# Kernel tuning notes

Hardware: AMD Instinct MI355X
Metric: run time of the kernel (lower is better)

Reference implementation:

```python
import jax, jax.numpy as jnp
import numpy as np

B, T, F, H, M = 64, 512, 32, 512, 20
O = (F + 2) * M  # (n_features + 2) * num_mixtures = 680


def _lstm_cell(x, h, c, w_ih, w_hh, b_ih, b_hh):
    # torch.nn.LSTMCell: gates ordered [i, f, g, o]
    gates = x @ w_ih.T + h @ w_hh.T + b_ih + b_hh
    i, f, g, o = jnp.split(gates, 4, axis=-1)
    i = jax.nn.sigmoid(i)
    f = jax.nn.sigmoid(f)
    g = jnp.tanh(g)
    o = jax.nn.sigmoid(o)
    c_new = f * c + i * g
    h_new = o * jnp.tanh(c_new)
    return h_new, c_new


def setup_inputs() -> dict:
    key = jax.random.key(0)
    ks = jax.random.split(key, 9)
    s1 = 1.0 / np.sqrt(H)  # torch LSTMCell init: U(-1/sqrt(hidden), 1/sqrt(hidden))
    s2 = 1.0 / np.sqrt(O)
    u = lambda k, shape, s: jax.random.uniform(k, shape, jnp.float32, -s, s)
    return {
        "data": jax.random.normal(ks[0], (B, T * F), jnp.float32),
        "W_ih1": u(ks[1], (4 * H, F), s1),
        "W_hh1": u(ks[2], (4 * H, H), s1),
        "b_ih1": u(ks[3], (4 * H,), s1),
        "b_hh1": u(ks[4], (4 * H,), s1),
        "W_ih2": u(ks[5], (4 * O, H), s2),
        "W_hh2": u(ks[6], (4 * O, O), s2),
        "b_ih2": u(ks[7], (4 * O,), s2),
        "b_hh2": u(ks[8], (4 * O,), s2),
    }


def reference(data, W_ih1, W_hh1, b_ih1, b_hh1, W_ih2, W_hh2, b_ih2, b_hh2):
    n_feat = W_ih1.shape[1]
    hid = W_hh1.shape[1]
    out_dim = W_hh2.shape[1]
    batch = data.shape[0]
    t_steps = data.shape[1] // n_feat
    xs = data.reshape(batch, t_steps, n_feat).transpose(1, 0, 2)  # (T, B, F)

    h1 = jnp.zeros((batch, hid), data.dtype)
    c1 = jnp.zeros((batch, hid), data.dtype)
    h2 = jnp.zeros((batch, out_dim), data.dtype)
    c2 = jnp.zeros((batch, out_dim), data.dtype)

    def step(carry, x_t):
        h1, c1, h2, c2 = carry
        h1, c1 = _lstm_cell(x_t, h1, c1, W_ih1, W_hh1, b_ih1, b_hh1)
        # NOTE: original feeds lstm1's CELL state c1 into lstm2, and collects
        # lstm2's CELL state (`output`) as the per-step output.
        h2, c2 = _lstm_cell(c1, h2, c2, W_ih2, W_hh2, b_ih2, b_hh2)
        return (h1, c1, h2, c2), c2

    _, outs = jax.lax.scan(step, (h1, c1, h2, c2), xs)  # (T, B, O)
    return outs.transpose(1, 0, 2)  # (B, T, O), matches torch.stack(outputs, 1)
```

## Files before the change

### kernel.cpp

```cpp
#include <hip/hip_runtime.h>
#include <math.h>

#define BB 64
#define TT 512
#define FF 32
#define HH 512
#define OO 680

typedef _Float16 half8 __attribute__((ext_vector_type(8)));
typedef float f32x4 __attribute__((ext_vector_type(4)));

#define H1SLAB 65536u
#define C1SLAB 65536u
#define H2SLAB 90112u
#define H1S_OFF 0u
#define C1S_OFF 131072u
#define H2S_OFF 262144u
#define BAR_OFF 442368u
#define MEMSET_BYTES 444928u

#define L1B  16
#define NBLK 59
#define LDS_BYTES 159744u

__device__ __forceinline__ float sigf(float x) { return 1.f / (1.f + expf(-x)); }

__device__ __forceinline__ unsigned long long aload8(const void* p) {
    return __hip_atomic_load((const unsigned long long*)p, __ATOMIC_RELAXED, __HIP_MEMORY_SCOPE_AGENT);
}
__device__ __forceinline__ void astore8(void* p, unsigned long long v) {
    __hip_atomic_store((unsigned long long*)p, v, __ATOMIC_RELAXED, __HIP_MEMORY_SCOPE_AGENT);
}
__device__ __forceinline__ half8 ld_act(const char* p) {
    union { unsigned long long u[2]; half8 h; } t;
    t.u[0] = aload8(p); t.u[1] = aload8(p + 8);
    return t.h;
}
__device__ __forceinline__ unsigned pack2h(float a, float b) {
    union { _Float16 h[2]; unsigned u; } t;
    t.h[0] = (_Float16)a; t.h[1] = (_Float16)b; return t.u;
}
__device__ __forceinline__ unsigned long long pack4h(float a, float b, float c, float d) {
    union { _Float16 h[4]; unsigned long long u; } t;
    t.h[0] = (_Float16)a; t.h[1] = (_Float16)b; t.h[2] = (_Float16)c; t.h[3] = (_Float16)d;
    return t.u;
}

__device__ __forceinline__ void gridbar(unsigned* bar, int blk, unsigned gen) {
    __syncthreads();
    if (threadIdx.x == 0) {
        const int x = blk & 7;
        const unsigned gsz = (x < 3) ? 8u : 7u;
        unsigned* cnt = bar + x * 32;
        const unsigned a = __hip_atomic_fetch_add(cnt, 1u, __ATOMIC_RELAXED, __HIP_MEMORY_SCOPE_AGENT);
        if (a == gen * gsz - 1u)
            __hip_atomic_store(bar + 256 + x * 32, gen, __ATOMIC_RELAXED, __HIP_MEMORY_SCOPE_AGENT);
        for (;;) {
            unsigned ok = 1u;
            #pragma unroll
            for (int r = 0; r < 8; ++r)
                ok &= (__hip_atomic_load(bar + 256 + r * 32, __ATOMIC_RELAXED, __HIP_MEMORY_SCOPE_AGENT) >= gen) ? 1u : 0u;
            if (ok) break;
            __builtin_amdgcn_s_sleep(1);
        }
    }
    __syncthreads();
}

#define MFMA4(B, AT) \
    acc0 = __builtin_amdgcn_mfma_f32_16x16x32_f16(*(const half8*)((AT)       ), (B), acc0, 0, 0, 0); \
    acc1 = __builtin_amdgcn_mfma_f32_16x16x32_f16(*(const half8*)((AT) + 1024), (B), acc1, 0, 0, 0); \
    acc2 = __builtin_amdgcn_mfma_f32_16x16x32_f16(*(const half8*)((AT) + 2048), (B), acc2, 0, 0, 0); \
    acc3 = __builtin_amdgcn_mfma_f32_16x16x32_f16(*(const half8*)((AT) + 3072), (B), acc3, 0, 0, 0);

__global__ __launch_bounds__(512, 1)
void rnn_mfma(const float* __restrict__ data,
    const float* __restrict__ Wih1, const float* __restrict__ Whh1,
    const float* __restrict__ bih1, const float* __restrict__ bhh1,
    const float* __restrict__ Wih2, const float* __restrict__ Whh2,
    const float* __restrict__ bih2, const float* __restrict__ bhh2,
    char* __restrict__ wsb, float* __restrict__ out)
{
    extern __shared__ char lds[];
    const int tid = threadIdx.x, wv = tid >> 6, l = tid & 63;
    const int hi = l >> 4, lo = l & 15;
    const int blk = blockIdx.x;
    const bool isL1 = blk < L1B;
    unsigned* bar = (unsigned*)(wsb + BAR_OFF);
    const int bfrag = wv & 3;
    const int b = bfrag * 16 + lo;
    const int c0 = isL1 ? blk * 32 : (blk - L1B) * 16;

    if (isL1) {
        for (int u = tid; u < 136 * 256; u += 512) {
            const int tile = u >> 8, w = u & 255;
            const int ll = w >> 2, jj = w & 3;
            const int ks = tile >> 3, rest = tile & 7;
            const int gate = rest >> 1, chi = rest & 1;
            const int col = c0 + chi * 16 + (ll & 15);
            const int row = gate * HH + col;
            const int kk = ks * 32 + (ll >> 4) * 8 + jj * 2;
            const float v0 = (kk < FF)     ? Wih1[(size_t)row * FF + kk]     : Whh1[(size_t)row * HH + kk - FF];
            const float v1 = (kk + 1 < FF) ? Wih1[(size_t)row * FF + kk + 1] : Whh1[(size_t)row * HH + kk + 1 - FF];
            ((unsigned*)lds)[tile * 256 + w] = pack2h(v0, v1);
        }
    } else {
        for (int u = tid; u < 152 * 256; u += 512) {
            const int tile = u >> 8, w = u & 255;
            const int ll = w >> 2, jj = w & 3;
            const int ks = tile >> 2, gate = tile & 3;
            const int col = c0 + (ll & 15);
            const int kk = ks * 32 + (ll >> 4) * 8 + jj * 2;
            float v0 = 0.f, v1 = 0.f;
            if (col < OO) {
                if (kk < HH) v0 = Wih2[((size_t)gate * OO + col) * HH + kk];
                else if (kk < 1192) v0 = Whh2[((size_t)gate * OO + col) * OO + kk - HH];
                if (kk + 1 < HH) v1 = Wih2[((size_t)gate * OO + col) * HH + kk + 1];
                else if (kk + 1 < 1192) v1 = Whh2[((size_t)gate * OO + col) * OO + kk + 1 - HH];
            }
            ((unsigned*)lds)[tile * 256 + w] = pack2h(v0, v1);
        }
    }
    __syncthreads();

    float bs[2][4][4];
    if (wv < 4) {
        if (isL1) {
            #pragma unroll
            for (int chi = 0; chi < 2; ++chi)
                #pragma unroll
                for (int r = 0; r < 4; ++r) {
                    const int col = c0 + chi * 16 + hi * 4 + r;
                    #pragma unroll
                    for (int g = 0; g < 4; ++g)
                        bs[chi][r][g] = bih1[g * HH + col] + bhh1[g * HH + col];
                }
        } else {
            #pragma unroll
            for (int r = 0; r < 4; ++r) {
                const int col = c0 + hi * 4 + r;
                const bool ok = col < OO;
                #pragma unroll
                for (int g = 0; g < 4; ++g)
                    bs[0][r][g] = ok ? (bih2[g * OO + col] + bhh2[g * OO + col]) : 0.f;
            }
        }
    }

    const int gh = wv >> 2;
    float cr[8] = {0.f,0.f,0.f,0.f,0.f,0.f,0.f,0.f};
    f32x4 (*part1)[4][64] = (f32x4(*)[4][64])(lds + 136 * 1024);
    f32x4* part2 = (f32x4*)(lds + 152 * 1024);

    f32x4 pend = {0,0,0,0};
    float* pendP = nullptr;

    for (int s = 0; s <= TT; ++s) {
        const int A = s & 1, Bx = A ^ 1;
        const bool active = isL1 ? (s < TT) : (s >= 1);
        f32x4 acc0 = {0,0,0,0}, acc1 = {0,0,0,0}, acc2 = {0,0,0,0}, acc3 = {0,0,0,0};

        if (active) {
            if (isL1) {
                {
                    const float* xp = data + (size_t)b * (TT * FF) + (size_t)s * FF + hi * 8;
                    const float4 xa = *(const float4*)xp;
                    const float4 xb = *(const float4*)(xp + 4);
                    half8 bxf;
                    bxf[0] = (_Float16)xa.x; bxf[1] = (_Float16)xa.y;
                    bxf[2] = (_Float16)xa.z; bxf[3] = (_Float16)xa.w;
                    bxf[4] = (_Float16)xb.x; bxf[5] = (_Float16)xb.y;
                    bxf[6] = (_Float16)xb.z; bxf[7] = (_Float16)xb.w;
                    const char* at = lds + (size_t)(gh * 4) * 1024 + (size_t)l * 16;
                    MFMA4(bxf, at);
                }
                const char* h1p = wsb + H1S_OFF + (size_t)A * H1SLAB + (size_t)l * 16;
                #pragma unroll
                for (int ks = 1; ks <= 16; ++ks) {
                    const half8 bf = ld_act(h1p + (size_t)(((ks - 1) * 4 + bfrag)) * 1024);
                    const char* at = lds + (size_t)(ks * 8 + gh * 4) * 1024 + (size_t)l * 16;
                    MFMA4(bf, at);
                }
            } else {
                if (gh == 0) {
                    if (pendP) { __builtin_nontemporal_store(pend, (f32x4*)pendP); pendP = nullptr; }
                    const char* c1p = wsb + C1S_OFF + (size_t)A * C1SLAB + (size_t)l * 16;
                    #pragma unroll
                    for (int ks = 0; ks < 16; ++ks) {
                        const half8 bf = ld_act(c1p + (size_t)(ks * 4 + bfrag) * 1024);
                        const char* at = lds + (size_t)ks * 4096 + (size_t)l * 16;
                        MFMA4(bf, at);
                    }
                    const char* h2p = wsb + H2S_OFF + (size_t)Bx * H2SLAB + (size_t)l * 16;
                    #pragma unroll
                    for (int ks = 16; ks < 19; ++ks) {
                        const half8 bf = ld_act(h2p + (size_t)((ks - 16) * 4 + bfrag) * 1024);
                        const char* at = lds + (size_t)ks * 4096 + (size_t)l * 16;
                        MFMA4(bf, at);
                    }
                } else {
                    const char* h2p = wsb + H2S_OFF + (size_t)Bx * H2SLAB + (size_t)l * 16;
                    #pragma unroll
                    for (int ks = 19; ks < 38; ++ks) {
                        const half8 bf = ld_act(h2p + (size_t)((ks - 16) * 4 + bfrag) * 1024);
                        const char* at = lds + (size_t)ks * 4096 + (size_t)l * 16;
                        MFMA4(bf, at);
                    }
                }
            }
        }

        if (isL1) {
            if (active) {
                if (wv >= 4) {
                    part1[wv - 4][0][l] = acc0; part1[wv - 4][1][l] = acc1;
                    part1[wv - 4][2][l] = acc2; part1[wv - 4][3][l] = acc3;
                }
                __syncthreads();
                if (wv < 4) {
                    #pragma unroll
                    for (int chi = 0; chi < 2; ++chi) {
                        const f32x4 o0 = (chi == 0) ? acc0 : acc1;
                        const f32x4 o1 = (chi == 0) ? acc2 : acc3;
                        const f32x4 p0 = part1[wv][chi][l];
                        const f32x4 p1 = part1[wv][2 + chi][l];
                        float cn[4], hn[4];
                        #pragma unroll
                        for (int r = 0; r < 4; ++r) {
                            const float ig = sigf(o0[r] + bs[chi][r][0]);
                            const float fg = sigf(o1[r] + bs[chi][r][1]);
                            const float gg = tanhf(p0[r] + bs[chi][r][2]);
                            const float og = sigf(p1[r] + bs[chi][r][3]);
                            const float c = fg * cr[chi * 4 + r] + ig * gg;
                            cr[chi * 4 + r] = c;
                            cn[r] = c; hn[r] = og * tanhf(c);
                        }
                        const int cc = c0 + chi * 16 + hi * 4;
                        const size_t aoff = (size_t)(((cc >> 5) * 4 + wv)) * 1024
                                          + (size_t)((((cc >> 3) & 3) * 16 + lo)) * 16
                                          + (size_t)((hi & 1) * 8);
                        astore8(wsb + H1S_OFF + (size_t)Bx * H1SLAB + aoff, pack4h(hn[0], hn[1], hn[2], hn[3]));
                        astore8(wsb + C1S_OFF + (size_t)Bx * C1SLAB + aoff, pack4h(cn[0], cn[1], cn[2], cn[3]));
                    }
                }
            }
        } else {
            if (active) {
                f32x4 pr0 = {0,0,0,0}, pr1 = {0,0,0,0}, pr2 = {0,0,0,0}, pr3 = {0,0,0,0};
                if (wv >= 4) part2[(wv - 4) * 64 + l] = acc0;
                __syncthreads();
                if (wv < 4) pr0 = part2[wv * 64 + l];
                __syncthreads();
                if (wv >= 4) part2[(wv - 4) * 64 + l] = acc1;
                __syncthreads();
                if (wv < 4) pr1 = part2[wv * 64 + l];
                __syncthreads();
                if (wv >= 4) part2[(wv - 4) * 64 + l] = acc2;
                __syncthreads();
                if (wv < 4) pr2 = part2[wv * 64 + l];
                __syncthreads();
                if (wv >= 4) part2[(wv - 4) * 64 + l] = acc3;
                __syncthreads();
                if (wv < 4) pr3 = part2[wv * 64 + l];
                if (wv < 4) {
                    const int u = s - 1;
                    float cn[4], hn[4];
                    #pragma unroll
                    for (int r = 0; r < 4; ++r) {
                        const float ig = sigf(acc0[r] + pr0[r] + bs[0][r][0]);
                        const float fg = sigf(acc1[r] + pr1[r] + bs[0][r][1]);
                        const float gg = tanhf(acc2[r] + pr2[r] + bs[0][r][2]);
                        const float og = sigf(acc3[r] + pr3[r] + bs[0][r][3]);
                        const float c = fg * cr[r] + ig * gg;
                        cr[r] = c;
                        cn[r] = c; hn[r] = og * tanhf(c);
                    }
                    const int cc = c0 + hi * 4;
                    if (cc < OO) {
                        pend[0] = cn[0]; pend[1] = cn[1]; pend[2] = cn[2]; pend[3] = cn[3];
                        pendP = out + (size_t)b * (TT * OO) + (size_t)u * OO + cc;
                        const size_t aoff = (size_t)(((cc >> 5) * 4 + wv)) * 1024
                                          + (size_t)((((cc >> 3) & 3) * 16 + lo)) * 16
                                          + (size_t)((hi & 1) * 8);
                        astore8(wsb + H2S_OFF + (size_t)A * H2SLAB + aoff, pack4h(hn[0], hn[1], hn[2], hn[3]));
                    }
                }
            }
        }
        gridbar(bar, blk, (unsigned)(s + 1));
    }

    if (!isL1 && wv < 4 && pendP)
        __builtin_nontemporal_store(pend, (f32x4*)pendP);
}

extern "C" void kernel_launch(void* const* d_in, const int* in_sizes, int n_in,
                              void* d_out, int out_size, void* d_ws, size_t ws_size,
                              hipStream_t stream)
{
    const float* data = (const float*)d_in[0];
    const float* Wih1 = (const float*)d_in[1];
    const float* Whh1 = (const float*)d_in[2];
    const float* bih1 = (const float*)d_in[3];
    const float* bhh1 = (const float*)d_in[4];
    const float* Wih2 = (const float*)d_in[5];
    const float* Whh2 = (const float*)d_in[6];
    const float* bih2 = (const float*)d_in[7];
    const float* bhh2 = (const float*)d_in[8];
    float* out = (float*)d_out;
    char* wsb  = (char*)d_ws;

    hipFuncSetAttribute((const void*)rnn_mfma, hipFuncAttributeMaxDynamicSharedMemorySize, (int)LDS_BYTES);
    hipMemsetAsync(wsb, 0, MEMSET_BYTES, stream);
    rnn_mfma<<<NBLK, 512, LDS_BYTES, stream>>>(data,
                                               Wih1, Whh1, bih1, bhh1,
                                               Wih2, Whh2, bih2, bhh2,
                                               wsb, out);
}
```

Baseline: 4.895 ms.

## Replace global grid barrier with layer-wise flag sync and 4-deep c1 ring

Replaces the per-step grid-wide barrier with separate producer/consumer counters and flags for layer-1 and layer-2 blocks. Layer 1 can now run up to three steps ahead of layer 2 through a 4-deep ring buffer for c1. Blocks shrink to 256 threads, so each wave does the full K reduction itself and the LDS partial-sum exchange with its extra __syncthreads is gone. The aim is to cut barrier latency and intra-block sync overhead on the serial recurrence, at the cost of more serial MFMA work per wave and busy-wait spinning without sleep.

Measured after the change: 4.495 ms. 8.2% less time.

```diff
diff --git a/kernel.cpp b/kernel.cpp
--- a/kernel.cpp
+++ b/kernel.cpp
@@ -15,13 +15,18 @@
 #define H2SLAB 90112u
 #define H1S_OFF 0u
 #define C1S_OFF 131072u
-#define H2S_OFF 262144u
-#define BAR_OFF 442368u
-#define MEMSET_BYTES 444928u
+#define H2S_OFF 393216u
+#define BAR_OFF 573440u
+#define MEMSET_BYTES 576000u
 
 #define L1B  16
 #define NBLK 59
-#define LDS_BYTES 159744u
+#define LDS_BYTES 155648u
+
+#define L1CNT(g) ((g)*32)
+#define L1FLG    64
+#define L2CNT(g) (96 + (g)*32)
+#define L2FLG    352
 
 __device__ __forceinline__ float sigf(float x) { return 1.f / (1.f + expf(-x)); }
 
@@ -30,6 +35,9 @@
 }
 __device__ __forceinline__ void astore8(void* p, unsigned long long v) {
     __hip_atomic_store((unsigned long long*)p, v, __ATOMIC_RELAXED, __HIP_MEMORY_SCOPE_AGENT);
+}
+__device__ __forceinline__ void astore32(unsigned* p, unsigned v) {
+    __hip_atomic_store(p, v, __ATOMIC_RELAXED, __HIP_MEMORY_SCOPE_AGENT);
 }
 __device__ __forceinline__ half8 ld_act(const char* p) {
     union { unsigned long long u[2]; half8 h; } t;
@@ -45,35 +53,29 @@
     t.h[0] = (_Float16)a; t.h[1] = (_Float16)b; t.h[2] = (_Float16)c; t.h[3] = (_Float16)d;
     return t.u;
 }
-
-__device__ __forceinline__ void gridbar(unsigned* bar, int blk, unsigned gen) {
-    __syncthreads();
-    if (threadIdx.x == 0) {
-        const int x = blk & 7;
-        const unsigned gsz = (x < 3) ? 8u : 7u;
-        unsigned* cnt = bar + x * 32;
-        const unsigned a = __hip_atomic_fetch_add(cnt, 1u, __ATOMIC_RELAXED, __HIP_MEMORY_SCOPE_AGENT);
-        if (a == gen * gsz - 1u)
-            __hip_atomic_store(bar + 256 + x * 32, gen, __ATOMIC_RELAXED, __HIP_MEMORY_SCOPE_AGENT);
-        for (;;) {
-            unsigned ok = 1u;
-            #pragma unroll
-            for (int r = 0; r < 8; ++r)
-                ok &= (__hip_atomic_load(bar + 256 + r * 32, __ATOMIC_RELAXED, __HIP_MEMORY_SCOPE_AGENT) >= gen) ? 1u : 0u;
-            if (ok) break;
-            __builtin_amdgcn_s_sleep(1);
-        }
-    }
-    __syncthreads();
-}
-
-#define MFMA4(B, AT) \
-    acc0 = __builtin_amdgcn_mfma_f32_16x16x32_f16(*(const half8*)((AT)       ), (B), acc0, 0, 0, 0); \
-    acc1 = __builtin_amdgcn_mfma_f32_16x16x32_f16(*(const half8*)((AT) + 1024), (B), acc1, 0, 0, 0); \
-    acc2 = __builtin_amdgcn_mfma_f32_16x16x32_f16(*(const half8*)((AT) + 2048), (B), acc2, 0, 0, 0); \
-    acc3 = __builtin_amdgcn_mfma_f32_16x16x32_f16(*(const half8*)((AT) + 3072), (B), acc3, 0, 0, 0);
-
-__global__ __launch_bounds__(512, 1)
+__device__ __forceinline__ unsigned minL1(const unsigned* bar) {
+    const unsigned long long v = aload8(bar + L1FLG);
+    const unsigned a = (unsigned)v, b = (unsigned)(v >> 32);
+    return a < b ? a : b;
+}
+__device__ __forceinline__ unsigned minL2(const unsigned* bar) {
+    const unsigned long long v0 = aload8(bar + L2FLG);
+    const unsigned long long v1 = aload8(bar + L2FLG + 2);
+    const unsigned long long v2 = aload8(bar + L2FLG + 4);
+    const unsigned long long v3 = aload8(bar + L2FLG + 6);
+    unsigned m = (unsigned)v0;
+    unsigned x;
+    x = (unsigned)(v0 >> 32); m = x < m ? x : m;
+    x = (unsigned)v1;         m = x < m ? x : m;
+    x = (unsigned)(v1 >> 32); m = x < m ? x : m;
+    x = (unsigned)v2;         m = x < m ? x : m;
+    x = (unsigned)(v2 >> 32); m = x < m ? x : m;
+    x = (unsigned)v3;         m = x < m ? x : m;
+    x = (unsigned)(v3 >> 32); m = x < m ? x : m;
+    return m;
+}
+
+__global__ __launch_bounds__(256, 1)
 void rnn_mfma(const float* __restrict__ data,
     const float* __restrict__ Wih1, const float* __restrict__ Whh1,
     const float* __restrict__ bih1, const float* __restrict__ bhh1,
@@ -85,14 +87,13 @@
     const int tid = threadIdx.x, wv = tid >> 6, l = tid & 63;
     const int hi = l >> 4, lo = l & 15;
     const int blk = blockIdx.x;
-    const bool isL1 = blk < L1B;
     unsigned* bar = (unsigned*)(wsb + BAR_OFF);
-    const int bfrag = wv & 3;
+    const int bfrag = wv;
     const int b = bfrag * 16 + lo;
-    const int c0 = isL1 ? blk * 32 : (blk - L1B) * 16;
-
-    if (isL1) {
-        for (int u = tid; u < 136 * 256; u += 512) {
+
+    if (blk < L1B) {
+        const int c0 = blk * 32;
+        for (int u = tid; u < 136 * 256; u += 256) {
             const int tile = u >> 8, w = u & 255;
             const int ll = w >> 2, jj = w & 3;
             const int ks = tile >> 3, rest = tile & 7;
@@ -104,8 +105,86 @@
             const float v1 = (kk + 1 < FF) ? Wih1[(size_t)row * FF + kk + 1] : Whh1[(size_t)row * HH + kk + 1 - FF];
             ((unsigned*)lds)[tile * 256 + w] = pack2h(v0, v1);
         }
+        __syncthreads();
+
+        float bs[2][4][4];
+        #pragma unroll
+        for (int chi = 0; chi < 2; ++chi)
+            #pragma unroll
+            for (int r = 0; r < 4; ++r) {
+                const int col = c0 + chi * 16 + hi * 4 + r;
+                #pragma unroll
+                for (int g = 0; g < 4; ++g)
+                    bs[chi][r][g] = bih1[g * HH + col] + bhh1[g * HH + col];
+            }
+        float cr[8] = {0.f,0.f,0.f,0.f,0.f,0.f,0.f,0.f};
+
+        for (int s = 0; s < TT; ++s) {
+            const int pr = s & 1;
+            const float* xp = data + (size_t)b * (TT * FF) + (size_t)s * FF + hi * 8;
+            const float4 xa = *(const float4*)xp;
+            const float4 xb4 = *(const float4*)(xp + 4);
+            if (s > 0) {
+                if (tid == 0) { while (minL1(bar) < (unsigned)s) {} }
+                __syncthreads();
+            }
+            half8 bx;
+            bx[0] = (_Float16)xa.x; bx[1] = (_Float16)xa.y; bx[2] = (_Float16)xa.z; bx[3] = (_Float16)xa.w;
+            bx[4] = (_Float16)xb4.x; bx[5] = (_Float16)xb4.y; bx[6] = (_Float16)xb4.z; bx[7] = (_Float16)xb4.w;
+
+            f32x4 acc[8];
+            #pragma unroll
+            for (int a = 0; a < 8; ++a) acc[a] = (f32x4){0.f,0.f,0.f,0.f};
+            #pragma unroll
+            for (int a = 0; a < 8; ++a)
+                acc[a] = __builtin_amdgcn_mfma_f32_16x16x32_f16(*(const half8*)(lds + (size_t)a * 1024 + (size_t)l * 16), bx, acc[a], 0, 0, 0);
+            const char* h1p = wsb + H1S_OFF + (size_t)pr * H1SLAB + (size_t)l * 16;
+            #pragma unroll
+            for (int ks = 1; ks <= 16; ++ks) {
+                const half8 bf = ld_act(h1p + (size_t)((ks - 1) * 4 + bfrag) * 1024);
+                #pragma unroll
+                for (int a = 0; a < 8; ++a)
+                    acc[a] = __builtin_amdgcn_mfma_f32_16x16x32_f16(*(const half8*)(lds + (size_t)(ks * 8 + a) * 1024 + (size_t)l * 16), bf, acc[a], 0, 0, 0);
+            }
+            if (s > 3) {
+                if (tid == 0) { while (minL2(bar) < (unsigned)(s - 3)) {} }
+                __syncthreads();
+            }
+            char* h1w = wsb + H1S_OFF + (size_t)(pr ^ 1) * H1SLAB;
+            char* c1w = wsb + C1S_OFF + (size_t)(s & 3) * C1SLAB;
+            #pragma unroll
+            for (int chi = 0; chi < 2; ++chi) {
+                const int cc = c0 + chi * 16 + hi * 4;
+                float cn[4], hn[4];
+                #pragma unroll
+                for (int r = 0; r < 4; ++r) {
+                    const float ig = sigf(acc[0 + chi][r] + bs[chi][r][0]);
+                    const float fg = sigf(acc[2 + chi][r] + bs[chi][r][1]);
+                    const float gg = tanhf(acc[4 + chi][r] + bs[chi][r][2]);
+                    const float og = sigf(acc[6 + chi][r] + bs[chi][r][3]);
+                    const float c = fg * cr[chi * 4 + r] + ig * gg;
+                    cr[chi * 4 + r] = c;
+                    cn[r] = c; hn[r] = og * tanhf(c);
+                }
+                const size_t aoff = (size_t)((cc >> 5) * 4 + bfrag) * 1024
+                                  + (size_t)((((cc >> 3) & 3) * 16 + lo)) * 16
+                                  + (size_t)(cc & 7) * 2;
+                astore8(h1w + aoff, pack4h(hn[0], hn[1], hn[2], hn[3]));
+                astore8(c1w + aoff, pack4h(cn[0], cn[1], cn[2], cn[3]));
+            }
+            __syncthreads();
+            if (tid == 0) {
+                const int g = blk & 1;
+                const unsigned e = (unsigned)(s + 1);
+                const unsigned a2 = __hip_atomic_fetch_add(bar + L1CNT(g), 1u, __ATOMIC_RELAXED, __HIP_MEMORY_SCOPE_AGENT);
+                if (a2 == e * 8u - 1u) astore32(bar + L1FLG + g, e);
+            }
+        }
     } else {
-        for (int u = tid; u < 152 * 256; u += 512) {
+        const int idx = blk - L1B, c0 = idx * 16;
+        const int grp = idx & 7;
+        const unsigned gsz = (grp < 3) ? 6u : 5u;
+        for (int u = tid; u < 152 * 256; u += 256) {
             const int tile = u >> 8, w = u & 255;
             const int ll = w >> 2, jj = w & 3;
             const int ks = tile >> 2, gate = tile & 3;
@@ -120,178 +199,78 @@
             }
             ((unsigned*)lds)[tile * 256 + w] = pack2h(v0, v1);
         }
+        __syncthreads();
+
+        const int cc = c0 + hi * 4;
+        float bs[4][4];
+        #pragma unroll
+        for (int r = 0; r < 4; ++r) {
+            const int col = cc + r;
+            const bool ok = col < OO;
+            #pragma unroll
+            for (int g = 0; g < 4; ++g)
+                bs[r][g] = ok ? (bih2[g * OO + col] + bhh2[g * OO + col]) : 0.f;
+        }
+        float cr[4] = {0.f,0.f,0.f,0.f};
+
+        for (int t = 1; t <= TT; ++t) {
+            if (tid == 0) { while (minL1(bar) < (unsigned)t) {} }
+            __syncthreads();
+            const char* c1p = wsb + C1S_OFF + (size_t)((t - 1) & 3) * C1SLAB + (size_t)l * 16;
+            half8 bcs[16];
+            #pragma unroll
+            for (int ks = 0; ks < 16; ++ks) bcs[ks] = ld_act(c1p + (size_t)(ks * 4 + bfrag) * 1024);
+            if (t > 1) {
+                if (tid == 0) { while (minL2(bar) < (unsigned)(t - 1)) {} }
+                __syncthreads();
+            }
+            const char* h2p = wsb + H2S_OFF + (size_t)((t & 1) ^ 1) * H2SLAB + (size_t)l * 16;
+            half8 bhs[22];
+            #pragma unroll
+            for (int ks = 0; ks < 22; ++ks) bhs[ks] = ld_act(h2p + (size_t)(ks * 4 + bfrag) * 1024);
+            f32x4 acc[4];
+            #pragma unroll
+            for (int g = 0; g < 4; ++g) acc[g] = (f32x4){0.f,0.f,0.f,0.f};
+            #pragma unroll
+            for (int ks = 0; ks < 16; ++ks) {
+                #pragma unroll
+                for (int g = 0; g < 4; ++g)
+                    acc[g] = __builtin_amdgcn_mfma_f32_16x16x32_f16(*(const half8*)(lds + (size_t)(ks * 4 + g) * 1024 + (size_t)l * 16), bcs[ks], acc[g], 0, 0, 0);
+            }
+            #pragma unroll
+            for (int ks = 0; ks < 22; ++ks) {
+                #pragma unroll
+                for (int g = 0; g < 4; ++g)
+                    acc[g] = __builtin_amdgcn_mfma_f32_16x16x32_f16(*(const half8*)(lds + (size_t)((16 + ks) * 4 + g) * 1024 + (size_t)l * 16), bhs[ks], acc[g], 0, 0, 0);
+            }
+            if (cc < OO) {
+                const int u_ = t - 1;
+                float cn[4], hn[4];
+                #pragma unroll
+                for (int r = 0; r < 4; ++r) {
+                    const float ig = sigf(acc[0][r] + bs[r][0]);
+                    const float fg = sigf(acc[1][r] + bs[r][1]);
+                    const float gg = tanhf(acc[2][r] + bs[r][2]);
+                    const float og = sigf(acc[3][r] + bs[r][3]);
+                    const float c = fg * cr[r] + ig * gg;
+                    cr[r] = c;
+                    cn[r] = c; hn[r] = og * tanhf(c);
+                }
+                const f32x4 q = {cn[0], cn[1], cn[2], cn[3]};
+                __builtin_nontemporal_store(q, (f32x4*)(out + (size_t)b * (TT * OO) + (size_t)u_ * OO + cc));
+                char* h2w = wsb + H2S_OFF + (size_t)(t & 1) * H2SLAB;
+                const size_t aoff = (size_t)((cc >> 5) * 4 + bfrag) * 1024
+                                  + (size_t)((((cc >> 3) & 3) * 16 + lo)) * 16
+                                  + (size_t)(cc & 7) * 2;
+                astore8(h2w + aoff, pack4h(hn[0], hn[1], hn[2], hn[3]));
+            }
+            __syncthreads();
+            if (t < TT && tid == 0) {
+                const unsigned a2 = __hip_atomic_fetch_add(bar + L2CNT(grp), 1u, __ATOMIC_RELAXED, __HIP_MEMORY_SCOPE_AGENT);
+                if (a2 == (unsigned)t * gsz - 1u) astore32(bar + L2FLG + grp, (unsigned)t);
+            }
+        }
     }
-    __syncthreads();
-
-    float bs[2][4][4];
-    if (wv < 4) {
-        if (isL1) {
-            #pragma unroll
-            for (int chi = 0; chi < 2; ++chi)
-                #pragma unroll
-                for (int r = 0; r < 4; ++r) {
-                    const int col = c0 + chi * 16 + hi * 4 + r;
-                    #pragma unroll
-                    for (int g = 0; g < 4; ++g)
-                        bs[chi][r][g] = bih1[g * HH + col] + bhh1[g * HH + col];
-                }
-        } else {
-            #pragma unroll
-            for (int r = 0; r < 4; ++r) {
-                const int col = c0 + hi * 4 + r;
-                const bool ok = col < OO;
-                #pragma unroll
-                for (int g = 0; g < 4; ++g)
-                    bs[0][r][g] = ok ? (bih2[g * OO + col] + bhh2[g * OO + col]) : 0.f;
-            }
-        }
-    }
-
-    const int gh = wv >> 2;
-    float cr[8] = {0.f,0.f,0.f,0.f,0.f,0.f,0.f,0.f};
-    f32x4 (*part1)[4][64] = (f32x4(*)[4][64])(lds + 136 * 1024);
-    f32x4* part2 = (f32x4*)(lds + 152 * 1024);
-
-    f32x4 pend = {0,0,0,0};
-    float* pendP = nullptr;
-
-    for (int s = 0; s <= TT; ++s) {
-        const int A = s & 1, Bx = A ^ 1;
-        const bool active = isL1 ? (s < TT) : (s >= 1);
-        f32x4 acc0 = {0,0,0,0}, acc1 = {0,0,0,0}, acc2 = {0,0,0,0}, acc3 = {0,0,0,0};
-
-        if (active) {
-            if (isL1) {
-                {
-                    const float* xp = data + (size_t)b * (TT * FF) + (size_t)s * FF + hi * 8;
-                    const float4 xa = *(const float4*)xp;
-                    const float4 xb = *(const float4*)(xp + 4);
-                    half8 bxf;
-                    bxf[0] = (_Float16)xa.x; bxf[1] = (_Float16)xa.y;
-                    bxf[2] = (_Float16)xa.z; bxf[3] = (_Float16)xa.w;
-                    bxf[4] = (_Float16)xb.x; bxf[5] = (_Float16)xb.y;
-                    bxf[6] = (_Float16)xb.z; bxf[7] = (_Float16)xb.w;
-                    const char* at = lds + (size_t)(gh * 4) * 1024 + (size_t)l * 16;
-                    MFMA4(bxf, at);
-                }
-                const char* h1p = wsb + H1S_OFF + (size_t)A * H1SLAB + (size_t)l * 16;
-                #pragma unroll
-                for (int ks = 1; ks <= 16; ++ks) {
-                    const half8 bf = ld_act(h1p + (size_t)(((ks - 1) * 4 + bfrag)) * 1024);
-                    const char* at = lds + (size_t)(ks * 8 + gh * 4) * 1024 + (size_t)l * 16;
-                    MFMA4(bf, at);
-                }
-            } else {
-                if (gh == 0) {
-                    if (pendP) { __builtin_nontemporal_store(pend, (f32x4*)pendP); pendP = nullptr; }
-                    const char* c1p = wsb + C1S_OFF + (size_t)A * C1SLAB + (size_t)l * 16;
-                    #pragma unroll
-                    for (int ks = 0; ks < 16; ++ks) {
-                        const half8 bf = ld_act(c1p + (size_t)(ks * 4 + bfrag) * 1024);
-                        const char* at = lds + (size_t)ks * 4096 + (size_t)l * 16;
-                        MFMA4(bf, at);
-                    }
-                    const char* h2p = wsb + H2S_OFF + (size_t)Bx * H2SLAB + (size_t)l * 16;
-                    #pragma unroll
-                    for (int ks = 16; ks < 19; ++ks) {
-                        const half8 bf = ld_act(h2p + (size_t)((ks - 16) * 4 + bfrag) * 1024);
-                        const char* at = lds + (size_t)ks * 4096 + (size_t)l * 16;
-                        MFMA4(bf, at);
-                    }
-                } else {
-                    const char* h2p = wsb + H2S_OFF + (size_t)Bx * H2SLAB + (size_t)l * 16;
-                    #pragma unroll
-                    for (int ks = 19; ks < 38; ++ks) {
-                        const half8 bf = ld_act(h2p + (size_t)((ks - 16) * 4 + bfrag) * 1024);
-                        const char* at = lds + (size_t)ks * 4096 + (size_t)l * 16;
-                        MFMA4(bf, at);
-                    }
-                }
-            }
-        }
-
-        if (isL1) {
-            if (active) {
-                if (wv >= 4) {
-                    part1[wv - 4][0][l] = acc0; part1[wv - 4][1][l] = acc1;
-                    part1[wv - 4][2][l] = acc2; part1[wv - 4][3][l] = acc3;
-                }
-                __syncthreads();
-                if (wv < 4) {
-                    #pragma unroll
-                    for (int chi = 0; chi < 2; ++chi) {
-                        const f32x4 o0 = (chi == 0) ? acc0 : acc1;
-                        const f32x4 o1 = (chi == 0) ? acc2 : acc3;
-                        const f32x4 p0 = part1[wv][chi][l];
-                        const f32x4 p1 = part1[wv][2 + chi][l];
-                        float cn[4], hn[4];
-                        #pragma unroll
-                        for (int r = 0; r < 4; ++r) {
-                            const float ig = sigf(o0[r] + bs[chi][r][0]);
-                            const float fg = sigf(o1[r] + bs[chi][r][1]);
-                            const float gg = tanhf(p0[r] + bs[chi][r][2]);
-                            const float og = sigf(p1[r] + bs[chi][r][3]);
-                            const float c = fg * cr[chi * 4 + r] + ig * gg;
-                            cr[chi * 4 + r] = c;
-                            cn[r] = c; hn[r] = og * tanhf(c);
-                        }
-                        const int cc = c0 + chi * 16 + hi * 4;
-                        const size_t aoff = (size_t)(((cc >> 5) * 4 + wv)) * 1024
-                                          + (size_t)((((cc >> 3) & 3) * 16 + lo)) * 16
-                                          + (size_t)((hi & 1) * 8);
-                        astore8(wsb + H1S_OFF + (size_t)Bx * H1SLAB + aoff, pack4h(hn[0], hn[1], hn[2], hn[3]));
-                        astore8(wsb + C1S_OFF + (size_t)Bx * C1SLAB + aoff, pack4h(cn[0], cn[1], cn[2], cn[3]));
-                    }
-                }
-            }
-        } else {
-            if (active) {
-                f32x4 pr0 = {0,0,0,0}, pr1 = {0,0,0,0}, pr2 = {0,0,0,0}, pr3 = {0,0,0,0};
-                if (wv >= 4) part2[(wv - 4) * 64 + l] = acc0;
-                __syncthreads();
-                if (wv < 4) pr0 = part2[wv * 64 + l];
-                __syncthreads();
-                if (wv >= 4) part2[(wv - 4) * 64 + l] = acc1;
-                __syncthreads();
-                if (wv < 4) pr1 = part2[wv * 64 + l];
-                __syncthreads();
-                if (wv >= 4) part2[(wv - 4) * 64 + l] = acc2;
-                __syncthreads();
-                if (wv < 4) pr2 = part2[wv * 64 + l];
-                __syncthreads();
-                if (wv >= 4) part2[(wv - 4) * 64 + l] = acc3;
-                __syncthreads();
-                if (wv < 4) pr3 = part2[wv * 64 + l];
-                if (wv < 4) {
-                    const int u = s - 1;
-                    float cn[4], hn[4];
-                    #pragma unroll
-                    for (int r = 0; r < 4; ++r) {
-                        const float ig = sigf(acc0[r] + pr0[r] + bs[0][r][0]);
-                        const float fg = sigf(acc1[r] + pr1[r] + bs[0][r][1]);
-                        const float gg = tanhf(acc2[r] + pr2[r] + bs[0][r][2]);
-                        const float og = sigf(acc3[r] + pr3[r] + bs[0][r][3]);
-                        const float c = fg * cr[r] + ig * gg;
-                        cr[r] = c;
-                        cn[r] = c; hn[r] = og * tanhf(c);
-                    }
-                    const int cc = c0 + hi * 4;
-                    if (cc < OO) {
-                        pend[0] = cn[0]; pend[1] = cn[1]; pend[2] = cn[2]; pend[3] = cn[3];
-                        pendP = out + (size_t)b * (TT * OO) + (size_t)u * OO + cc;
-                        const size_t aoff = (size_t)(((cc >> 5) * 4 + wv)) * 1024
-                                          + (size_t)((((cc >> 3) & 3) * 16 + lo)) * 16
-                                          + (size_t)((hi & 1) * 8);
-                        astore8(wsb + H2S_OFF + (size_t)A * H2SLAB + aoff, pack4h(hn[0], hn[1], hn[2], hn[3]));
-                    }
-                }
-            }
-        }
-        gridbar(bar, blk, (unsigned)(s + 1));
-    }
-
-    if (!isL1 && wv < 4 && pendP)
-        __builtin_nontemporal_store(pend, (f32x4*)pendP);
 }
 
 extern "C" void kernel_launch(void* const* d_in, const int* in_sizes, int n_in,
@@ -312,7 +291,7 @@
 
     hipFuncSetAttribute((const void*)rnn_mfma, hipFuncAttributeMaxDynamicSharedMemorySize, (int)LDS_BYTES);
     hipMemsetAsync(wsb, 0, MEMSET_BYTES, stream);
-    rnn_mfma<<<NBLK, 512, LDS_BYTES, stream>>>(data,
+    rnn_mfma<<<NBLK, 256, LDS_BYTES, stream>>>(data,
                                                Wih1, Whh1, bih1, bhh1,
                                                Wih2, Whh2, bih2, bhh2,
                                                wsb, out);
```
